# Optimization experiments

Hardware: AMD Instinct MI355X
Metric: run time of the kernel (lower is better)

The kernel has to match this reference:

```python
import jax, jax.numpy as jnp
import numpy as np

N_NODES = 250_000
N_EDGES = 1_250_000
N_CRY = 50_000
EMB = 200
FEA = 64
HID = 256
N_GRAPH = 3
ELEM_HEADS = 3
CRY_HEADS = 3


def _simple_net(x, w1, b1, w2, b2):
    # SimpleNetwork([d_in, 256, d_out]): Linear -> LeakyReLU -> Linear
    h = jax.nn.leaky_relu(x @ w1 + b1, negative_slope=0.01)
    return h @ w2 + b2


def setup_inputs() -> dict:
    key = jax.random.key(0)
    ks = jax.random.split(key, 32)
    s = 0.05
    inp = {
        # weights strictly positive (fractional stoichiometry weights)
        "elem_weights": jax.random.uniform(ks[0], (N_NODES, 1), jnp.float32) * 0.9 + 0.05,
        "elem_fea": jax.random.normal(ks[1], (N_NODES, EMB), jnp.float32),
        "self_fea_idx": jax.random.randint(ks[2], (N_EDGES,), 0, N_NODES),
        "nbr_fea_idx": jax.random.randint(ks[3], (N_EDGES,), 0, N_NODES),
        "cry_elem_idx": jnp.sort(jax.random.randint(ks[4], (N_NODES,), 0, N_CRY)),
        # embedding: Linear(EMB, FEA-1)
        "emb_w": jax.random.normal(ks[5], (EMB, FEA - 1), jnp.float32) * s,
        "emb_b": jnp.zeros((FEA - 1,), jnp.float32),
        # graph-layer attention heads (n_graph, elem_heads, ...)
        "g_gate_w1": jax.random.normal(ks[6], (N_GRAPH, ELEM_HEADS, 2 * FEA, HID), jnp.float32) * s,
        "g_gate_b1": jnp.zeros((N_GRAPH, ELEM_HEADS, HID), jnp.float32),
        "g_gate_w2": jax.random.normal(ks[7], (N_GRAPH, ELEM_HEADS, HID, 1), jnp.float32) * s,
        "g_gate_b2": jnp.zeros((N_GRAPH, ELEM_HEADS, 1), jnp.float32),
        "g_msg_w1": jax.random.normal(ks[8], (N_GRAPH, ELEM_HEADS, 2 * FEA, HID), jnp.float32) * s,
        "g_msg_b1": jnp.zeros((N_GRAPH, ELEM_HEADS, HID), jnp.float32),
        "g_msg_w2": jax.random.normal(ks[9], (N_GRAPH, ELEM_HEADS, HID, FEA), jnp.float32) * s,
        "g_msg_b2": jnp.zeros((N_GRAPH, ELEM_HEADS, FEA), jnp.float32),
        "g_pow": jax.random.normal(ks[10], (N_GRAPH, ELEM_HEADS), jnp.float32),
        # crystal pooling heads
        "c_gate_w1": jax.random.normal(ks[11], (CRY_HEADS, FEA, HID), jnp.float32) * s,
        "c_gate_b1": jnp.zeros((CRY_HEADS, HID), jnp.float32),
        "c_gate_w2": jax.random.normal(ks[12], (CRY_HEADS, HID, 1), jnp.float32) * s,
        "c_gate_b2": jnp.zeros((CRY_HEADS, 1), jnp.float32),
        "c_msg_w1": jax.random.normal(ks[13], (CRY_HEADS, FEA, HID), jnp.float32) * s,
        "c_msg_b1": jnp.zeros((CRY_HEADS, HID), jnp.float32),
        "c_msg_w2": jax.random.normal(ks[14], (CRY_HEADS, HID, FEA), jnp.float32) * s,
        "c_msg_b2": jnp.zeros((CRY_HEADS, FEA), jnp.float32),
        "c_pow": jax.random.normal(ks[15], (CRY_HEADS,), jnp.float32),
    }
    return inp


def _attn_pool(fea, weights, index, num_segments, gw1, gb1, gw2, gb2, mw1, mb1, mw2, mb2, p):
    # WeightedAttentionPooling: scatter-softmax with (weights ** pow) factor
    gate = _simple_net(fea, gw1, gb1, gw2, gb2)                       # (E, 1)
    gmax = jax.ops.segment_max(gate, index, num_segments=num_segments)
    gate = (weights ** p) * jnp.exp(gate - gmax[index])
    den = jax.ops.segment_sum(gate, index, num_segments=num_segments)
    gate = gate / (den[index] + 1e-10)
    msg = _simple_net(fea, mw1, mb1, mw2, mb2)                        # (E, FEA)
    return jax.ops.segment_sum(gate * msg, index, num_segments=num_segments)


def reference(elem_weights, elem_fea, self_fea_idx, nbr_fea_idx, cry_elem_idx,
              emb_w, emb_b,
              g_gate_w1, g_gate_b1, g_gate_w2, g_gate_b2,
              g_msg_w1, g_msg_b1, g_msg_w2, g_msg_b2, g_pow,
              c_gate_w1, c_gate_b1, c_gate_w2, c_gate_b2,
              c_msg_w1, c_msg_b1, c_msg_w2, c_msg_b2, c_pow):
    n = elem_fea.shape[0]
    x = elem_fea @ emb_w + emb_b                                      # (N, FEA-1)
    x = jnp.concatenate([x, elem_weights], axis=1)                    # (N, FEA)
    w_nbr = elem_weights[nbr_fea_idx]                                 # (M, 1)
    for l in range(g_pow.shape[0]):
        fea = jnp.concatenate([x[self_fea_idx], x[nbr_fea_idx]], axis=1)  # (M, 2*FEA)
        heads = []
        for h in range(g_pow.shape[1]):
            heads.append(_attn_pool(
                fea, w_nbr, self_fea_idx, n,
                g_gate_w1[l, h], g_gate_b1[l, h], g_gate_w2[l, h], g_gate_b2[l, h],
                g_msg_w1[l, h], g_msg_b1[l, h], g_msg_w2[l, h], g_msg_b2[l, h],
                g_pow[l, h]))
        x = jnp.mean(jnp.stack(heads), axis=0) + x                    # residual
    heads = []
    for h in range(c_pow.shape[0]):
        heads.append(_attn_pool(
            x, elem_weights, cry_elem_idx, N_CRY,
            c_gate_w1[h], c_gate_b1[h], c_gate_w2[h], c_gate_b2[h],
            c_msg_w1[h], c_msg_b1[h], c_msg_w2[h], c_msg_b2[h],
            c_pow[h]))
    return jnp.mean(jnp.stack(heads), axis=0)                         # (C, FEA)
```

## Files before the change

### kernel.cpp

```cpp
#include <hip/hip_runtime.h>
#include <math.h>

#define NN 250000
#define NE 1250000
#define NC 50000
#define EMBD 200
#define NCH_E 245
#define NCH_C 49
#define NBLK 22000
#define NCBLK 6000
#define SSTR  ((size_t)NBLK * 64)
#define SSTRC ((size_t)NCBLK * 64)

typedef unsigned int u32;
typedef unsigned short u16;
typedef short s16x8 __attribute__((ext_vector_type(8)));
typedef float f32x4 __attribute__((ext_vector_type(4)));

__device__ __forceinline__ u16 f2bf(float f) {
    u32 u = __float_as_uint(f);
    return (u16)((u + 0x7FFFu + ((u >> 16) & 1u)) >> 16);
}
__device__ __forceinline__ float bf2f(u16 u) { return __uint_as_float(((u32)u) << 16); }
__device__ __forceinline__ u32 cvtpk(float lo, float hi) {
    u32 r;
    asm("v_cvt_pk_bf16_f32 %0, %1, %2" : "=v"(r) : "v"(lo), "v"(hi));
    return r;
}
__device__ __forceinline__ float lrelu(float v) { return v > 0.f ? v : 0.01f * v; }

__global__ void k_pack(const float* __restrict__ src, u16* __restrict__ dst,
                       int K, int N, int nheads)
{
    const int t = blockIdx.x * 256 + threadIdx.x;
    const int F = (K / 32) * (N / 16);
    if (t >= nheads * F * 64) return;
    const int lane = t & 63;
    const int fh = t >> 6;
    const int f = fh % F, head = fh / F;
    const int ng = f % (N / 16), ks = f / (N / 16);
    const int q = lane >> 4, c = lane & 15;
    const float* s = src + (size_t)head * K * N;
    u16 o[8];
    #pragma unroll
    for (int i = 0; i < 8; ++i)
        o[i] = f2bf(s[(size_t)(32 * ks + 8 * q + i) * N + 16 * ng + c]);
    uint4 v;
    v.x = (u32)o[0] | ((u32)o[1] << 16);
    v.y = (u32)o[2] | ((u32)o[3] << 16);
    v.z = (u32)o[4] | ((u32)o[5] << 16);
    v.w = (u32)o[6] | ((u32)o[7] << 16);
    *(uint4*)(dst + (size_t)head * K * N + ((size_t)f * 64 + lane) * 8) = v;
}

__global__ void k_packe(const float* __restrict__ src, u16* __restrict__ dst)
{
    const int t = blockIdx.x * 256 + threadIdx.x;
    if (t >= 28 * 64) return;
    const int lane = t & 63, f = t >> 6;
    const int ng = f & 3, ks = f >> 2;
    const int q = lane >> 4, c = lane & 15;
    u16 o[8];
    #pragma unroll
    for (int i = 0; i < 8; ++i) {
        const int kr = 32 * ks + 8 * q + i;
        const int col = 16 * ng + c;
        o[i] = (kr < EMBD && col < 63) ? f2bf(src[kr * 63 + col]) : (u16)0;
    }
    uint4 v;
    v.x = (u32)o[0] | ((u32)o[1] << 16);
    v.y = (u32)o[2] | ((u32)o[3] << 16);
    v.z = (u32)o[4] | ((u32)o[5] << 16);
    v.w = (u32)o[6] | ((u32)o[7] << 16);
    *(uint4*)(dst + ((size_t)f * 64 + lane) * 8) = v;
}

__global__ void k_pack2(const float* __restrict__ src, u16* __restrict__ dst, int nheads)
{
    const int t = blockIdx.x * 256 + threadIdx.x;
    const int F = 32;
    if (t >= nheads * F * 64) return;
    const int lane = t & 63;
    const int fh = t >> 6;
    const int f = fh % F, head = fh / F;
    const int ks2 = f >> 2, ng = f & 3;
    const int q = lane >> 4, c = lane & 15;
    const int half = ks2 >> 2, k2l = ks2 & 3;
    const float* s = src + (size_t)head * 256 * 64;
    u16 o[8];
    #pragma unroll
    for (int i = 0; i < 8; ++i) {
        const int pl = 32 * k2l + 8 * q + i;
        const int krow = (pl >> 5) * 64 + (2 * half + (pl & 1)) * 16 + ((pl >> 1) & 15);
        o[i] = f2bf(s[(size_t)krow * 64 + 16 * ng + c]);
    }
    uint4 v;
    v.x = (u32)o[0] | ((u32)o[1] << 16);
    v.y = (u32)o[2] | ((u32)o[3] << 16);
    v.z = (u32)o[4] | ((u32)o[5] << 16);
    v.w = (u32)o[6] | ((u32)o[7] << 16);
    *(uint4*)(dst + (size_t)head * 256 * 64 + ((size_t)f * 64 + lane) * 8) = v;
}

__global__ void k_packg(const float* __restrict__ src, u16* __restrict__ dst, int nheads)
{
    const int t = blockIdx.x * 256 + threadIdx.x;
    if (t >= nheads * 8 * 64) return;
    const int lane = t & 63;
    const int fh = t >> 6;
    const int f = fh & 7, head = fh >> 3;
    const int half = f >> 2, k2l = f & 3;
    const int q = lane >> 4;
    u16 o[8];
    #pragma unroll
    for (int i = 0; i < 8; ++i) {
        const int pl = 32 * k2l + 8 * q + i;
        const int krow = (pl >> 5) * 64 + (2 * half + (pl & 1)) * 16 + ((pl >> 1) & 15);
        o[i] = f2bf(src[head * 256 + krow]);
    }
    uint4 v;
    v.x = (u32)o[0] | ((u32)o[1] << 16);
    v.y = (u32)o[2] | ((u32)o[3] << 16);
    v.z = (u32)o[4] | ((u32)o[5] << 16);
    v.w = (u32)o[6] | ((u32)o[7] << 16);
    *(uint4*)(dst + ((size_t)(head * 8 + f) * 64 + lane) * 8) = v;
}

__global__ __launch_bounds__(256) void k_embed_mm(
    const float* __restrict__ elem_fea, const float* __restrict__ elem_w,
    const u16* __restrict__ webp, const float* __restrict__ emb_b,
    float* __restrict__ x, u16* __restrict__ xbf)
{
    __shared__ __align__(16) u16 Ahi[64 * 256];
    __shared__ __align__(16) u16 Alo[64 * 256];
    const int tid = threadIdx.x;
    const int n0 = blockIdx.x * 64;

    for (int i = tid; i < 64 * 3; i += 256) {
        const int row = i / 3, j = 25 + i % 3;
        uint4 z; z.x = 0; z.y = 0; z.z = 0; z.w = 0;
        *(uint4*)((char*)Ahi + row * 512 + ((j ^ (row & 7)) * 16)) = z;
        *(uint4*)((char*)Alo + row * 512 + ((j ^ (row & 7)) * 16)) = z;
    }
    for (int i = tid; i < 64 * 50; i += 256) {
        const int row = i / 50, f4 = i % 50;
        const int node = min(n0 + row, NN - 1);
        float4 v = *(const float4*)(elem_fea + (size_t)node * EMBD + f4 * 4);
        const u16 h0 = f2bf(v.x), h1 = f2bf(v.y), h2 = f2bf(v.z), h3 = f2bf(v.w);
        uint2 hi, lo;
        hi.x = (u32)h0 | ((u32)h1 << 16);
        hi.y = (u32)h2 | ((u32)h3 << 16);
        lo.x = (u32)f2bf(v.x - bf2f(h0)) | ((u32)f2bf(v.y - bf2f(h1)) << 16);
        lo.y = (u32)f2bf(v.z - bf2f(h2)) | ((u32)f2bf(v.w - bf2f(h3)) << 16);
        const int off = row * 512 + (((f4 >> 1) ^ (row & 7)) * 16) + (f4 & 1) * 8;
        *(uint2*)((char*)Ahi + off) = hi;
        *(uint2*)((char*)Alo + off) = lo;
    }
    __syncthreads();

    const int w = tid >> 6, lane = tid & 63, q = lane >> 4, c = lane & 15;
    s16x8 B[7];
    #pragma unroll
    for (int ks = 0; ks < 7; ++ks)
        B[ks] = *(const s16x8*)(webp + ((size_t)(ks * 4 + w) * 64 + lane) * 8);
    f32x4 acc[4];
    #pragma unroll
    for (int m = 0; m < 4; ++m) acc[m] = 0.f;
    #pragma unroll
    for (int ks = 0; ks < 7; ++ks) {
        #pragma unroll
        for (int m = 0; m < 4; ++m) {
            const int row = m * 16 + c;
            const int g = (ks * 4 + q) ^ (row & 7);
            s16x8 ah = *(const s16x8*)((const char*)Ahi + row * 512 + g * 16);
            s16x8 al = *(const s16x8*)((const char*)Alo + row * 512 + g * 16);
            acc[m] = __builtin_amdgcn_mfma_f32_16x16x32_bf16(ah, B[ks], acc[m], 0, 0, 0);
            acc[m] = __builtin_amdgcn_mfma_f32_16x16x32_bf16(al, B[ks], acc[m], 0, 0, 0);
        }
    }
    const int col = w * 16 + c;
    const float bv = (col < 63) ? emb_b[col] : 0.f;
    #pragma unroll
    for (int m = 0; m < 4; ++m)
        #pragma unroll
        for (int r = 0; r < 4; ++r) {
            const int node = n0 + m * 16 + q * 4 + r;
            if (node < NN) {
                const float val = (col < 63) ? acc[m][r] + bv : elem_w[node];
                x[(size_t)node * 64 + col] = val;
                xbf[(size_t)node * 64 + col] = f2bf(val);
            }
        }
}

__global__ void k_deg(const int* __restrict__ idx, int* __restrict__ deg, int n) {
    int e = blockIdx.x * 256 + threadIdx.x;
    if (e < n) atomicAdd(&deg[idx[e]], 1);
}

__global__ void k_nodepack(const int* __restrict__ deg, int* __restrict__ nstart,
                           int* __restrict__ ctotal, int total_n)
{
    __shared__ int sdeg[1024];
    __shared__ int sst[1024];
    const int c0 = blockIdx.x << 10;
    const int cnt = min(1024, total_n - c0);
    for (int i = threadIdx.x; i < cnt; i += 64) sdeg[i] = deg[c0 + i];
    __syncthreads();
    if (threadIdx.x == 0) {
        int cur = 0;
        for (int i = 0; i < cnt; ++i) {
            int d = sdeg[i];
            if (d > 0 && ((cur & 63) + d > 64)) cur = (cur + 63) & ~63;
            sst[i] = cur;
            cur += d;
        }
        ctotal[blockIdx.x] = (cur + 63) & ~63;
    }
    __syncthreads();
    for (int i = threadIdx.x; i < cnt; i += 64) nstart[c0 + i] = sst[i];
}

__global__ void k_chunkscan(const int* __restrict__ ctotal, int* __restrict__ cbase, int nch) {
    __shared__ int s[256];
    int t = threadIdx.x;
    int v = (t < nch) ? ctotal[t] : 0;
    s[t] = v;
    __syncthreads();
    for (int off = 1; off < 256; off <<= 1) {
        int add = (t >= off) ? s[t - off] : 0;
        __syncthreads();
        s[t] += add;
        __syncthreads();
    }
    if (t < nch) cbase[t] = s[t] - v;
}

__global__ void k_fill(const int* __restrict__ self_idx, const int* __restrict__ nbr_idx,
                       const float* __restrict__ elem_w,
                       const int* __restrict__ nstart, const int* __restrict__ cbase,
                       int* __restrict__ cursor, int2* __restrict__ gnode,
                       float* __restrict__ gwn)
{
    int e = blockIdx.x * 256 + threadIdx.x;
    if (e >= NE) return;
    int n = self_idx[e];
    int r = atomicAdd(&cursor[n], 1);
    int slot = cbase[n >> 10] + nstart[n] + r;
    int nb = nbr_idx[e];
    gnode[slot] = make_int2(n, nb);
    gwn[slot] = elem_w[nb];
}

__global__ void k_cfill(const int* __restrict__ cry_idx, const float* __restrict__ elem_w,
                        const int* __restrict__ nstart, const int* __restrict__ cbase,
                        int* __restrict__ cursor, int2* __restrict__ gnode,
                        float* __restrict__ gwn)
{
    int n = blockIdx.x * 256 + threadIdx.x;
    if (n >= NN) return;
    int cg = cry_idx[n];
    int r = atomicAdd(&cursor[cg], 1);
    int slot = cbase[cg >> 10] + nstart[cg] + r;
    gnode[slot] = make_int2(cg, n);
    gwn[slot] = elem_w[n];
}

template<int KD>
__global__ __launch_bounds__(256, 4) void k_lgate(
    const u16* __restrict__ xbf, const int2* __restrict__ gnode,
    const float* __restrict__ gwn,
    const u16* __restrict__ gw1p, const float* __restrict__ gb1,
    const u16* __restrict__ gw2p, const float* __restrict__ gpw,
    float* __restrict__ sgf_out, size_t sstr)
{
    constexpr int KS = KD / 32;
    constexpr int G  = KD / 8;
    constexpr int RB = KD * 2;
    __shared__ __align__(16) u16 sA[64 * KD];
    __shared__ __align__(16) u16 sH[64 * 128];
    __shared__ float sg[4][64];
    __shared__ float gfin[64], tval[64];
    __shared__ float swn[64];
    __shared__ int   snid[64];
    __shared__ short srs[64], sre[64];
    const int tid = threadIdx.x;
    const int base = blockIdx.x * 64;
    if (gnode[base].x < 0) return;

    if (tid < 64) {
        int2 nn = gnode[base + tid];
        snid[tid] = nn.x;
        swn[tid] = gwn[base + tid];
    }
    for (int i = tid; i < 64 * G; i += 256) {
        const int row = i / G, g = i % G;
        const int2 nn = gnode[base + row];
        const int node = (KD == 128) ? ((g < 8) ? nn.x : nn.y) : nn.y;
        uint4 v; v.x = 0; v.y = 0; v.z = 0; v.w = 0;
        if (node >= 0) v = *(const uint4*)(xbf + (size_t)node * 64 + (g & 7) * 8);
        *(uint4*)((char*)sA + row * RB + ((g ^ (row & 7)) * 16)) = v;
    }
    __syncthreads();
    if (tid < 64) {
        int n = snid[tid];
        int rs = tid, re = tid + 1;
        if (n >= 0) {
            while (rs > 0 && snid[rs - 1] == n) --rs;
            while (re < 64 && snid[re] == n) ++re;
        }
        srs[tid] = (short)rs; sre[tid] = (short)re;
    }

    const int w = tid >> 6, lane = tid & 63, q = lane >> 4, c = lane & 15;

    #pragma unroll 1
    for (int h = 0; h < 3; ++h) {
        f32x4 acc2[4];
        #pragma unroll
        for (int m = 0; m < 4; ++m) acc2[m] = 0.f;
        const u16* wp = gw1p + (size_t)h * KD * 256;
        #pragma unroll 1
        for (int half = 0; half < 2; ++half) {
            f32x4 acc[4][2];
            #pragma unroll
            for (int m = 0; m < 4; ++m) { acc[m][0] = 0.f; acc[m][1] = 0.f; }
            __builtin_amdgcn_s_setprio(1);
            #pragma unroll 2
            for (int ks = 0; ks < KS; ++ks) {
                s16x8 B1[2];
                #pragma unroll
                for (int n2 = 0; n2 < 2; ++n2)
                    B1[n2] = *(const s16x8*)(wp + ((size_t)(ks * 16 + w * 4 + half * 2 + n2) * 64 + lane) * 8);
                s16x8 a[4];
                #pragma unroll
                for (int m = 0; m < 4; ++m) {
                    const int row = m * 16 + c;
                    a[m] = *(const s16x8*)((const char*)sA + row * RB + (((ks * 4 + q) ^ (row & 7)) * 16));
                }
                #pragma unroll
                for (int n2 = 0; n2 < 2; ++n2)
                    #pragma unroll
                    for (int m = 0; m < 4; ++m)
                        acc[m][n2] = __builtin_amdgcn_mfma_f32_16x16x32_bf16(a[m], B1[n2], acc[m][n2], 0, 0, 0);
            }
            __builtin_amdgcn_s_setprio(0);

            __syncthreads();
            const float b1a = gb1[h * 256 + w * 64 + (half * 2 + 0) * 16 + c];
            const float b1b = gb1[h * 256 + w * 64 + (half * 2 + 1) * 16 + c];
            #pragma unroll
            for (int m = 0; m < 4; ++m)
                #pragma unroll
                for (int r = 0; r < 4; ++r) {
                    const int row = m * 16 + q * 4 + r;
                    const u32 pk = cvtpk(lrelu(acc[m][0][r] + b1a), lrelu(acc[m][1][r] + b1b));
                    *(u32*)((char*)sH + row * 256 + (((w * 4 + (c >> 2)) ^ (row & 7)) * 16) + (c & 3) * 4) = pk;
                }
            s16x8 B2 = *(const s16x8*)(gw2p + ((size_t)(h * 8 + half * 4 + w) * 64 + lane) * 8);
            __syncthreads();

            __builtin_amdgcn_s_setprio(1);
            #pragma unroll
            for (int m = 0; m < 4; ++m) {
                const int row = m * 16 + c;
                s16x8 a2 = *(const s16x8*)((const char*)sH + row * 256 + (((w * 4 + q) ^ (row & 7)) * 16));
                acc2[m] = __builtin_amdgcn_mfma_f32_16x16x32_bf16(a2, B2, acc2[m], 0, 0, 0);
            }
            __builtin_amdgcn_s_setprio(0);
        }
        if (c == 0) {
            #pragma unroll
            for (int m = 0; m < 4; ++m)
                #pragma unroll
                for (int r = 0; r < 4; ++r)
                    sg[w][m * 16 + q * 4 + r] = acc2[m][r];
        }
        __syncthreads();
        if (tid < 64)
            gfin[tid] = (snid[tid] >= 0) ? sg[0][tid] + sg[1][tid] + sg[2][tid] + sg[3][tid] : -1e30f;
        __syncthreads();
        if (tid < 64) {
            const int rs = srs[tid], re = sre[tid];
            float m = -1e30f;
            for (int j = rs; j < re; ++j) m = fmaxf(m, gfin[j]);
            tval[tid] = (snid[tid] >= 0) ? powf(swn[tid], gpw[h]) * expf(gfin[tid] - m) : 0.f;
        }
        __syncthreads();
        if (tid < 64) {
            const int rs = srs[tid], re = sre[tid];
            float d = 1e-10f;
            for (int j = rs; j < re; ++j) d += tval[j];
            sgf_out[sstr * h + base + tid] = tval[tid] / d;
        }
        __syncthreads();
    }
}

template<int KD, bool RESID>
__global__ __launch_bounds__(256, 4) void k_lmsg(
    const u16* __restrict__ xbf, const int2* __restrict__ gnode,
    const u16* __restrict__ mw1p, const float* __restrict__ mb1,
    const u16* __restrict__ mw2p, const float* __restrict__ mb2,
    const float* __restrict__ sgf_in, float* __restrict__ outp, size_t sstr)
{
    constexpr int KS = KD / 32;
    constexpr int G  = KD / 8;
    constexpr int RB = KD * 2;
    __shared__ __align__(16) u16 sA[64 * KD];
    __shared__ __align__(16) u16 sH[64 * 128];
    __shared__ float sgfl[64][3];
    __shared__ int   snid[64];
    __shared__ short srs[64], sre[64];
    const int tid = threadIdx.x;
    const int base = blockIdx.x * 64;
    if (gnode[base].x < 0) return;

    if (tid < 64) snid[tid] = gnode[base + tid].x;
    if (tid < 192) {
        const int row = tid / 3, h = tid % 3;
        sgfl[row][h] = sgf_in[sstr * h + base + row];
    }
    for (int i = tid; i < 64 * G; i += 256) {
        const int row = i / G, g = i % G;
        const int2 nn = gnode[base + row];
        const int node = (KD == 128) ? ((g < 8) ? nn.x : nn.y) : nn.y;
        uint4 v; v.x = 0; v.y = 0; v.z = 0; v.w = 0;
        if (node >= 0) v = *(const uint4*)(xbf + (size_t)node * 64 + (g & 7) * 8);
        *(uint4*)((char*)sA + row * RB + ((g ^ (row & 7)) * 16)) = v;
    }
    __syncthreads();
    if (tid < 64) {
        int n = snid[tid];
        int rs = tid, re = tid + 1;
        if (n >= 0) {
            while (rs > 0 && snid[rs - 1] == n) --rs;
            while (re < 64 && snid[re] == n) ++re;
        }
        srs[tid] = (short)rs; sre[tid] = (short)re;
    }

    const int w = tid >> 6, lane = tid & 63, q = lane >> 4, c = lane & 15;
    float wacc[4][4];
    #pragma unroll
    for (int m = 0; m < 4; ++m)
        #pragma unroll
        for (int r = 0; r < 4; ++r) wacc[m][r] = 0.f;

    #pragma unroll 1
    for (int h = 0; h < 3; ++h) {
        const u16* wp = mw1p + (size_t)h * KD * 256;
        #pragma unroll 1
        for (int half = 0; half < 2; ++half) {
            f32x4 acc[4][2];
            #pragma unroll
            for (int m = 0; m < 4; ++m) { acc[m][0] = 0.f; acc[m][1] = 0.f; }
            __builtin_amdgcn_s_setprio(1);
            #pragma unroll 2
            for (int ks = 0; ks < KS; ++ks) {
                s16x8 B1[2];
                #pragma unroll
                for (int n2 = 0; n2 < 2; ++n2)
                    B1[n2] = *(const s16x8*)(wp + ((size_t)(ks * 16 + w * 4 + half * 2 + n2) * 64 + lane) * 8);
                s16x8 a[4];
                #pragma unroll
                for (int m = 0; m < 4; ++m) {
                    const int row = m * 16 + c;
                    a[m] = *(const s16x8*)((const char*)sA + row * RB + (((ks * 4 + q) ^ (row & 7)) * 16));
                }
                #pragma unroll
                for (int n2 = 0; n2 < 2; ++n2)
                    #pragma unroll
                    for (int m = 0; m < 4; ++m)
                        acc[m][n2] = __builtin_amdgcn_mfma_f32_16x16x32_bf16(a[m], B1[n2], acc[m][n2], 0, 0, 0);
            }
            __builtin_amdgcn_s_setprio(0);

            __syncthreads();
            const float b1a = mb1[h * 256 + w * 64 + (half * 2 + 0) * 16 + c];
            const float b1b = mb1[h * 256 + w * 64 + (half * 2 + 1) * 16 + c];
            #pragma unroll
            for (int m = 0; m < 4; ++m)
                #pragma unroll
                for (int r = 0; r < 4; ++r) {
                    const int row = m * 16 + q * 4 + r;
                    const u32 pk = cvtpk(lrelu(acc[m][0][r] + b1a), lrelu(acc[m][1][r] + b1b));
                    *(u32*)((char*)sH + row * 256 + (((w * 4 + (c >> 2)) ^ (row & 7)) * 16) + (c & 3) * 4) = pk;
                }
            s16x8 B2[4];
            #pragma unroll
            for (int k2 = 0; k2 < 4; ++k2)
                B2[k2] = *(const s16x8*)(mw2p + (size_t)h * 256 * 64 + ((size_t)((half * 4 + k2) * 4 + w) * 64 + lane) * 8);
            __syncthreads();

            f32x4 acc2[4];
            #pragma unroll
            for (int m = 0; m < 4; ++m) acc2[m] = 0.f;
            __builtin_amdgcn_s_setprio(1);
            #pragma unroll
            for (int k2 = 0; k2 < 4; ++k2) {
                #pragma unroll
                for (int m2 = 0; m2 < 4; ++m2) {
                    const int row = m2 * 16 + c;
                    s16x8 a2 = *(const s16x8*)((const char*)sH + row * 256 + (((k2 * 4 + q) ^ (row & 7)) * 16));
                    acc2[m2] = __builtin_amdgcn_mfma_f32_16x16x32_bf16(a2, B2[k2], acc2[m2], 0, 0, 0);
                }
            }
            __builtin_amdgcn_s_setprio(0);
            const float b2v = half ? mb2[h * 64 + w * 16 + c] : 0.f;
            #pragma unroll
            for (int m2 = 0; m2 < 4; ++m2)
                #pragma unroll
                for (int r = 0; r < 4; ++r) {
                    const int row = m2 * 16 + q * 4 + r;
                    wacc[m2][r] += (acc2[m2][r] + b2v) * sgfl[row][h];
                }
        }
        __syncthreads();
    }

    float* waccL = (float*)sH;
    #pragma unroll
    for (int m = 0; m < 4; ++m)
        #pragma unroll
        for (int r = 0; r < 4; ++r)
            waccL[(m * 16 + q * 4 + r) * 64 + w * 16 + c] = wacc[m][r];
    __syncthreads();
    {
        const int col = tid & 63, grp = tid >> 6;
        for (int i = grp; i < 64; i += 4) {
            const int n = snid[i];
            if (n >= 0 && srs[i] == (short)i) {
                float s = 0.f;
                const int re = sre[i];
                for (int j = i; j < re; ++j) s += waccL[j * 64 + col];
                if (RESID) outp[(size_t)n * 64 + col] += s * (1.f / 3.f);
                else       outp[(size_t)n * 64 + col]  = s * (1.f / 3.f);
            }
        }
    }
}

__global__ void k_mirror(const float* __restrict__ x, u16* __restrict__ xbf, int n4)
{
    int i = blockIdx.x * 256 + threadIdx.x;
    if (i >= n4) return;
    float4 xv = *(const float4*)(x + (size_t)i * 4);
    uint2 o;
    o.x = cvtpk(xv.x, xv.y);
    o.y = cvtpk(xv.z, xv.w);
    *(uint2*)(xbf + (size_t)i * 4) = o;
}

extern "C" void kernel_launch(void* const* d_in, const int* in_sizes, int n_in,
                              void* d_out, int out_size, void* d_ws, size_t ws_size,
                              hipStream_t stream)
{
    const float* elem_w   = (const float*)d_in[0];
    const float* elem_fea = (const float*)d_in[1];
    const int*   self_idx = (const int*)d_in[2];
    const int*   nbr_idx  = (const int*)d_in[3];
    const int*   cry_idx  = (const int*)d_in[4];
    const float* emb_w    = (const float*)d_in[5];
    const float* emb_b    = (const float*)d_in[6];
    const float* gg_w1    = (const float*)d_in[7];
    const float* gg_b1    = (const float*)d_in[8];
    const float* gg_w2    = (const float*)d_in[9];
    const float* gm_w1    = (const float*)d_in[11];
    const float* gm_b1    = (const float*)d_in[12];
    const float* gm_w2    = (const float*)d_in[13];
    const float* gm_b2    = (const float*)d_in[14];
    const float* g_pow    = (const float*)d_in[15];
    const float* cg_w1    = (const float*)d_in[16];
    const float* cg_b1    = (const float*)d_in[17];
    const float* cg_w2    = (const float*)d_in[18];
    const float* cm_w1    = (const float*)d_in[20];
    const float* cm_b1    = (const float*)d_in[21];
    const float* cm_w2    = (const float*)d_in[22];
    const float* cm_b2    = (const float*)d_in[23];
    const float* c_pow    = (const float*)d_in[24];

    char* wsp = (char*)d_ws;
    size_t off = 0;
    auto alloc = [&](size_t b) { char* p = wsp + off; off += (b + 255) & ~(size_t)255; return p; };
    float* x      = (float*)alloc((size_t)NN * 64 * 4);
    u16*   xbf    = (u16*)  alloc((size_t)NN * 64 * 2);
    float* sgf    = (float*)alloc((size_t)3 * SSTR * 4);
    float* csgf   = (float*)alloc((size_t)3 * SSTRC * 4);
    int* deg    = (int*)alloc((size_t)NN * 4);
    int* nstart = (int*)alloc((size_t)NN * 4);
    int* cursor = (int*)alloc((size_t)NN * 4);
    int* ctotal = (int*)alloc((size_t)NCH_E * 4);
    int* cbase  = (int*)alloc((size_t)NCH_E * 4);
    int2* gnode = (int2*)alloc((size_t)NBLK * 64 * 8);
    float* gwn  = (float*)alloc((size_t)NBLK * 64 * 4);
    int* cdeg    = (int*)alloc((size_t)NC * 4);
    int* cnstart = (int*)alloc((size_t)NC * 4);
    int* ccursor = (int*)alloc((size_t)NC * 4);
    int* cctotal = (int*)alloc((size_t)NCH_C * 4);
    int* ccbase  = (int*)alloc((size_t)NCH_C * 4);
    int2* cgnode = (int2*)alloc((size_t)NCBLK * 64 * 8);
    float* cgwn  = (float*)alloc((size_t)NCBLK * 64 * 4);
    u16* wg1p = (u16*)alloc((size_t)9 * 128 * 256 * 2);
    u16* wm1p = (u16*)alloc((size_t)9 * 128 * 256 * 2);
    u16* wm2p = (u16*)alloc((size_t)9 * 256 * 64 * 2);
    u16* wg2p = (u16*)alloc((size_t)9 * 8 * 64 * 8 * 2);
    u16* cg1p = (u16*)alloc((size_t)3 * 64 * 256 * 2);
    u16* cm1p = (u16*)alloc((size_t)3 * 64 * 256 * 2);
    u16* cm2p = (u16*)alloc((size_t)3 * 256 * 64 * 2);
    u16* cg2p = (u16*)alloc((size_t)3 * 8 * 64 * 8 * 2);
    u16* webp = (u16*)alloc((size_t)224 * 64 * 2);

    auto pack = [&](const float* s, u16* d, int K, int N, int H) {
        int tot = H * (K / 32) * (N / 16) * 64;
        k_pack<<<(tot + 255) / 256, 256, 0, stream>>>(s, d, K, N, H);
    };
    pack(gg_w1, wg1p, 128, 256, 9);
    pack(gm_w1, wm1p, 128, 256, 9);
    pack(cg_w1, cg1p, 64, 256, 3);
    pack(cm_w1, cm1p, 64, 256, 3);
    k_pack2<<<(9 * 32 * 64 + 255) / 256, 256, 0, stream>>>(gm_w2, wm2p, 9);
    k_pack2<<<(3 * 32 * 64 + 255) / 256, 256, 0, stream>>>(cm_w2, cm2p, 3);
    k_packg<<<(9 * 8 * 64 + 255) / 256, 256, 0, stream>>>(gg_w2, wg2p, 9);
    k_packg<<<(3 * 8 * 64 + 255) / 256, 256, 0, stream>>>(cg_w2, cg2p, 3);
    k_packe<<<7, 256, 0, stream>>>(emb_w, webp);

    hipMemsetAsync(deg, 0, (size_t)NN * 4, stream);
    hipMemsetAsync(cursor, 0, (size_t)NN * 4, stream);
    hipMemsetAsync(gnode, 0xFF, (size_t)NBLK * 64 * 8, stream);
    k_deg<<<(NE + 255) / 256, 256, 0, stream>>>(self_idx, deg, NE);
    k_nodepack<<<NCH_E, 64, 0, stream>>>(deg, nstart, ctotal, NN);
    k_chunkscan<<<1, 256, 0, stream>>>(ctotal, cbase, NCH_E);
    k_fill<<<(NE + 255) / 256, 256, 0, stream>>>(self_idx, nbr_idx, elem_w,
                                                 nstart, cbase, cursor, gnode, gwn);
    hipMemsetAsync(cdeg, 0, (size_t)NC * 4, stream);
    hipMemsetAsync(ccursor, 0, (size_t)NC * 4, stream);
    hipMemsetAsync(cgnode, 0xFF, (size_t)NCBLK * 64 * 8, stream);
    k_deg<<<(NN + 255) / 256, 256, 0, stream>>>(cry_idx, cdeg, NN);
    k_nodepack<<<NCH_C, 64, 0, stream>>>(cdeg, cnstart, cctotal, NC);
    k_chunkscan<<<1, 256, 0, stream>>>(cctotal, ccbase, NCH_C);
    k_cfill<<<(NN + 255) / 256, 256, 0, stream>>>(cry_idx, elem_w,
                                                  cnstart, ccbase, ccursor, cgnode, cgwn);

    k_embed_mm<<<(NN + 63) / 64, 256, 0, stream>>>(elem_fea, elem_w, webp, emb_b, x, xbf);

    for (int l = 0; l < 3; ++l) {
        k_lgate<128><<<NBLK, 256, 0, stream>>>(
            xbf, gnode, gwn,
            wg1p + (size_t)l * 3 * 128 * 256, gg_b1 + l * 768,
            wg2p + (size_t)l * 3 * 8 * 64 * 8, g_pow + l * 3, sgf, SSTR);
        k_lmsg<128, true><<<NBLK, 256, 0, stream>>>(
            xbf, gnode,
            wm1p + (size_t)l * 3 * 128 * 256, gm_b1 + l * 768,
            wm2p + (size_t)l * 3 * 256 * 64, gm_b2 + l * 192, sgf, x, SSTR);
        k_mirror<<<(NN * 64 / 4 + 255) / 256, 256, 0, stream>>>(x, xbf, NN * 64 / 4);
    }

    hipMemsetAsync(d_out, 0, (size_t)NC * 64 * 4, stream);
    k_lgate<64><<<NCBLK, 256, 0, stream>>>(
        xbf, cgnode, cgwn, cg1p, cg_b1, cg2p, c_pow, csgf, SSTRC);
    k_lmsg<64, false><<<NCBLK, 256, 0, stream>>>(
        xbf, cgnode, cm1p, cm_b1, cm2p, cm_b2, csgf, (float*)d_out, SSTRC);
}
```

Baseline: 4.033 ms.

## Compute full hidden width per head in one pass to reuse A fragments

The first-layer GEMM in the gate and message kernels now accumulates all four N-subtiles per wave in a single K loop instead of two half passes. Each A fragment is read from LDS once per head rather than twice, and the loop overhead of the K sweep is halved. The cost is doubled accumulator registers, so launch bounds drop from 4 to 3 blocks per SM, which lowers occupancy. The per-head trailing barrier in the message kernel is also moved to after the head loop.

```diff
diff --git a/kernel.cpp b/kernel.cpp
--- a/kernel.cpp
+++ b/kernel.cpp
@@ -267,7 +267,7 @@
 }
 
 template<int KD>
-__global__ __launch_bounds__(256, 4) void k_lgate(
+__global__ __launch_bounds__(256, 3) void k_lgate(
     const u16* __restrict__ xbf, const int2* __restrict__ gnode,
     const float* __restrict__ gwn,
     const u16* __restrict__ gw1p, const float* __restrict__ gb1,
@@ -316,48 +316,49 @@
 
     #pragma unroll 1
     for (int h = 0; h < 3; ++h) {
+        const u16* wp = gw1p + (size_t)h * KD * 256;
+        f32x4 acc[4][4];
+        #pragma unroll
+        for (int m = 0; m < 4; ++m)
+            #pragma unroll
+            for (int n4 = 0; n4 < 4; ++n4) acc[m][n4] = 0.f;
+        __builtin_amdgcn_s_setprio(1);
+        #pragma unroll 2
+        for (int ks = 0; ks < KS; ++ks) {
+            s16x8 a[4];
+            #pragma unroll
+            for (int m = 0; m < 4; ++m) {
+                const int row = m * 16 + c;
+                a[m] = *(const s16x8*)((const char*)sA + row * RB + (((ks * 4 + q) ^ (row & 7)) * 16));
+            }
+            #pragma unroll
+            for (int n4 = 0; n4 < 4; ++n4) {
+                s16x8 B1 = *(const s16x8*)(wp + ((size_t)(ks * 16 + w * 4 + n4) * 64 + lane) * 8);
+                #pragma unroll
+                for (int m = 0; m < 4; ++m)
+                    acc[m][n4] = __builtin_amdgcn_mfma_f32_16x16x32_bf16(a[m], B1, acc[m][n4], 0, 0, 0);
+            }
+        }
+        __builtin_amdgcn_s_setprio(0);
+
         f32x4 acc2[4];
         #pragma unroll
         for (int m = 0; m < 4; ++m) acc2[m] = 0.f;
-        const u16* wp = gw1p + (size_t)h * KD * 256;
         #pragma unroll 1
-        for (int half = 0; half < 2; ++half) {
-            f32x4 acc[4][2];
-            #pragma unroll
-            for (int m = 0; m < 4; ++m) { acc[m][0] = 0.f; acc[m][1] = 0.f; }
-            __builtin_amdgcn_s_setprio(1);
-            #pragma unroll 2
-            for (int ks = 0; ks < KS; ++ks) {
-                s16x8 B1[2];
-                #pragma unroll
-                for (int n2 = 0; n2 < 2; ++n2)
-                    B1[n2] = *(const s16x8*)(wp + ((size_t)(ks * 16 + w * 4 + half * 2 + n2) * 64 + lane) * 8);
-                s16x8 a[4];
-                #pragma unroll
-                for (int m = 0; m < 4; ++m) {
-                    const int row = m * 16 + c;
-                    a[m] = *(const s16x8*)((const char*)sA + row * RB + (((ks * 4 + q) ^ (row & 7)) * 16));
-                }
-                #pragma unroll
-                for (int n2 = 0; n2 < 2; ++n2)
-                    #pragma unroll
-                    for (int m = 0; m < 4; ++m)
-                        acc[m][n2] = __builtin_amdgcn_mfma_f32_16x16x32_bf16(a[m], B1[n2], acc[m][n2], 0, 0, 0);
-            }
-            __builtin_amdgcn_s_setprio(0);
-
+        for (int h2 = 0; h2 < 2; ++h2) {
             __syncthreads();
-            const float b1a = gb1[h * 256 + w * 64 + (half * 2 + 0) * 16 + c];
-            const float b1b = gb1[h * 256 + w * 64 + (half * 2 + 1) * 16 + c];
+            const float b1a = gb1[h * 256 + w * 64 + (h2 * 2 + 0) * 16 + c];
+            const float b1b = gb1[h * 256 + w * 64 + (h2 * 2 + 1) * 16 + c];
             #pragma unroll
             for (int m = 0; m < 4; ++m)
                 #pragma unroll
                 for (int r = 0; r < 4; ++r) {
                     const int row = m * 16 + q * 4 + r;
-                    const u32 pk = cvtpk(lrelu(acc[m][0][r] + b1a), lrelu(acc[m][1][r] + b1b));
+                    const u32 pk = cvtpk(lrelu(acc[m][h2 * 2 + 0][r] + b1a),
+                                         lrelu(acc[m][h2 * 2 + 1][r] + b1b));
                     *(u32*)((char*)sH + row * 256 + (((w * 4 + (c >> 2)) ^ (row & 7)) * 16) + (c & 3) * 4) = pk;
                 }
-            s16x8 B2 = *(const s16x8*)(gw2p + ((size_t)(h * 8 + half * 4 + w) * 64 + lane) * 8);
+            s16x8 B2 = *(const s16x8*)(gw2p + ((size_t)(h * 8 + h2 * 4 + w) * 64 + lane) * 8);
             __syncthreads();
 
             __builtin_amdgcn_s_setprio(1);
@@ -398,7 +399,7 @@
 }
 
 template<int KD, bool RESID>
-__global__ __launch_bounds__(256, 4) void k_lmsg(
+__global__ __launch_bounds__(256, 3) void k_lmsg(
     const u16* __restrict__ xbf, const int2* __restrict__ gnode,
     const u16* __restrict__ mw1p, const float* __restrict__ mb1,
     const u16* __restrict__ mw2p, const float* __restrict__ mb2,
@@ -450,47 +451,48 @@
     #pragma unroll 1
     for (int h = 0; h < 3; ++h) {
         const u16* wp = mw1p + (size_t)h * KD * 256;
+        f32x4 acc[4][4];
+        #pragma unroll
+        for (int m = 0; m < 4; ++m)
+            #pragma unroll
+            for (int n4 = 0; n4 < 4; ++n4) acc[m][n4] = 0.f;
+        __builtin_amdgcn_s_setprio(1);
+        #pragma unroll 2
+        for (int ks = 0; ks < KS; ++ks) {
+            s16x8 a[4];
+            #pragma unroll
+            for (int m = 0; m < 4; ++m) {
+                const int row = m * 16 + c;
+                a[m] = *(const s16x8*)((const char*)sA + row * RB + (((ks * 4 + q) ^ (row & 7)) * 16));
+            }
+            #pragma unroll
+            for (int n4 = 0; n4 < 4; ++n4) {
+                s16x8 B1 = *(const s16x8*)(wp + ((size_t)(ks * 16 + w * 4 + n4) * 64 + lane) * 8);
+                #pragma unroll
+                for (int m = 0; m < 4; ++m)
+                    acc[m][n4] = __builtin_amdgcn_mfma_f32_16x16x32_bf16(a[m], B1, acc[m][n4], 0, 0, 0);
+            }
+        }
+        __builtin_amdgcn_s_setprio(0);
+
         #pragma unroll 1
-        for (int half = 0; half < 2; ++half) {
-            f32x4 acc[4][2];
-            #pragma unroll
-            for (int m = 0; m < 4; ++m) { acc[m][0] = 0.f; acc[m][1] = 0.f; }
-            __builtin_amdgcn_s_setprio(1);
-            #pragma unroll 2
-            for (int ks = 0; ks < KS; ++ks) {
-                s16x8 B1[2];
-                #pragma unroll
-                for (int n2 = 0; n2 < 2; ++n2)
-                    B1[n2] = *(const s16x8*)(wp + ((size_t)(ks * 16 + w * 4 + half * 2 + n2) * 64 + lane) * 8);
-                s16x8 a[4];
-                #pragma unroll
-                for (int m = 0; m < 4; ++m) {
-                    const int row = m * 16 + c;
-                    a[m] = *(const s16x8*)((const char*)sA + row * RB + (((ks * 4 + q) ^ (row & 7)) * 16));
-                }
-                #pragma unroll
-                for (int n2 = 0; n2 < 2; ++n2)
-                    #pragma unroll
-                    for (int m = 0; m < 4; ++m)
-                        acc[m][n2] = __builtin_amdgcn_mfma_f32_16x16x32_bf16(a[m], B1[n2], acc[m][n2], 0, 0, 0);
-            }
-            __builtin_amdgcn_s_setprio(0);
-
+        for (int h2 = 0; h2 < 2; ++h2) {
             __syncthreads();
-            const float b1a = mb1[h * 256 + w * 64 + (half * 2 + 0) * 16 + c];
-            const float b1b = mb1[h * 256 + w * 64 + (half * 2 + 1) * 16 + c];
+            const float b1a = mb1[h * 256 + w * 64 + (h2 * 2 + 0) * 16 + c];
+            const float b1b = mb1[h * 256 + w * 64 + (h2 * 2 + 1) * 16 + c];
             #pragma unroll
             for (int m = 0; m < 4; ++m)
                 #pragma unroll
                 for (int r = 0; r < 4; ++r) {
                     const int row = m * 16 + q * 4 + r;
-                    const u32 pk = cvtpk(lrelu(acc[m][0][r] + b1a), lrelu(acc[m][1][r] + b1b));
+                    const u32 pk = cvtpk(lrelu(acc[m][h2 * 2 + 0][r] + b1a),
+                                         lrelu(acc[m][h2 * 2 + 1][r] + b1b));
                     *(u32*)((char*)sH + row * 256 + (((w * 4 + (c >> 2)) ^ (row & 7)) * 16) + (c & 3) * 4) = pk;
                 }
             s16x8 B2[4];
             #pragma unroll
             for (int k2 = 0; k2 < 4; ++k2)
-                B2[k2] = *(const s16x8*)(mw2p + (size_t)h * 256 * 64 + ((size_t)((half * 4 + k2) * 4 + w) * 64 + lane) * 8);
+                B2[k2] = *(const s16x8*)(mw2p + (size_t)h * 256 * 64 + ((size_t)((h2 * 4 + k2) * 4 + w) * 64 + lane) * 8);
             __syncthreads();
 
             f32x4 acc2[4];
@@ -507,7 +509,7 @@
                 }
             }
             __builtin_amdgcn_s_setprio(0);
-            const float b2v = half ? mb2[h * 64 + w * 16 + c] : 0.f;
+            const float b2v = h2 ? mb2[h * 64 + w * 16 + c] : 0.f;
             #pragma unroll
             for (int m2 = 0; m2 < 4; ++m2)
                 #pragma unroll
@@ -516,8 +518,8 @@
                     wacc[m2][r] += (acc2[m2][r] + b2v) * sgfl[row][h];
                 }
         }
-        __syncthreads();
-    }
+    }
+    __syncthreads();
 
     float* waccL = (float*)sH;
     #pragma unroll
```

After: 9.651 ms. 139% more time.
